# Kernel optimization log

Measured on AMD Instinct MI355X. Metric: run time of the kernel, lower is better.

The kernel has to match this reference:

```python
import jax, jax.numpy as jnp
import numpy as np

B, T, C, NH = 2, 128, 384, 6
H = 768          # memory MLP hidden (expansion=2)
P, M = 4, 16     # persistent + long-term memory tokens; prefix_len = P+M
LR, MOM, DECAY = 0.01, 0.9, 0.001

def setup_inputs() -> dict:
    key = jax.random.key(0)
    ks = jax.random.split(key, 12)
    s = 0.02
    return {
        'x':          jax.random.normal(ks[0], (B, T, C), jnp.float32),
        'c_attn_w':   jax.random.normal(ks[1], (C, 3 * C), jnp.float32) * s,
        'c_attn_b':   jnp.zeros((3 * C,), jnp.float32),
        'c_proj_w':   jax.random.normal(ks[2], (C, C), jnp.float32) * s,
        'c_proj_b':   jnp.zeros((C,), jnp.float32),
        'ln1_g': jnp.ones((C,), jnp.float32), 'ln1_b': jnp.zeros((C,), jnp.float32),
        'ln2_g': jnp.ones((C,), jnp.float32), 'ln2_b': jnp.zeros((C,), jnp.float32),
        'fc_w':       jax.random.normal(ks[3], (C, 4 * C), jnp.float32) * s,
        'fc_b':       jnp.zeros((4 * C,), jnp.float32),
        'pr_w':       jax.random.normal(ks[4], (4 * C, C), jnp.float32) * s,
        'pr_b':       jnp.zeros((C,), jnp.float32),
        'mem_w1':     jax.random.normal(ks[5], (C, H), jnp.float32) * s,
        'mem_w2':     jax.random.normal(ks[6], (H, C), jnp.float32) * s,
        'wk':         jax.random.normal(ks[7], (C, C), jnp.float32) * s,
        'wv':         jax.random.normal(ks[8], (C, C), jnp.float32) * s,
        'mem_queries': jax.random.normal(ks[9], (M, C), jnp.float32) * s,
        'persist':    jax.random.normal(ks[10], (P, C), jnp.float32) * s,
    }

def _ln(x, g, b):
    mu = jnp.mean(x, -1, keepdims=True)
    var = jnp.mean((x - mu) ** 2, -1, keepdims=True)
    return (x - mu) * jax.lax.rsqrt(var + 1e-5) * g + b

def _scan_log(gates, tokens):
    # x[t] = gate[t]*x[t-1] + token[t] via log-cumsum trick (scan axis = 1)
    while gates.ndim < tokens.ndim:
        gates = gates[..., None]
    g = jnp.clip(gates, 1e-7, 1.0 - 1e-7)
    lc = jnp.cumsum(jnp.log(g), axis=1)
    return jnp.cumsum(tokens * jnp.exp(-lc), axis=1) * jnp.exp(lc)

def _forward(x, c_attn_w, c_attn_b, c_proj_w, c_proj_b, ln1_g, ln1_b, ln2_g, ln2_b,
             fc_w, fc_b, pr_w, pr_b, mem_w1, mem_w2, wk, wv, mem_queries, persist):
    b = x.shape[0]
    hd = C // NH
    PL = P + M
    xn = _ln(x, ln1_g, ln1_b)
    # --- retrieve long-term memory tokens with previous-segment memory weights ---
    retr = jax.nn.silu(mem_queries @ mem_w1) @ mem_w2              # [M, C]
    pref = jnp.concatenate([persist, retr], axis=0)                # [PL, C]
    seq = jnp.concatenate([jnp.broadcast_to(pref, (b, PL, C)), xn], axis=1)  # [b, t, C]
    t = seq.shape[1]
    # --- prefix-LM masked attention ---
    qkv = seq @ c_attn_w + c_attn_b
    q, k, v = jnp.split(qkv, 3, axis=-1)
    def heads(z):
        return z.reshape(b, t, NH, hd).transpose(0, 2, 1, 3)       # [b, nh, t, hd]
    q, k, v = heads(q), heads(k), heads(v)
    sc = jnp.einsum('bhqd,bhkd->bhqk', q, k) / np.float32(np.sqrt(hd))
    idx = jnp.arange(t)
    kp = idx < PL  # key in prefix
    # prefix_lm_mask: key_in_prefix OR (both in suffix AND causal)
    allowed = kp[None, :] | ((~kp[:, None]) & (~kp[None, :]) & (idx[:, None] >= idx[None, :]))
    sc = jnp.where(allowed, sc, -jnp.inf)
    y = jnp.einsum('bhqk,bhkd->bhqd', jax.nn.softmax(sc, axis=-1), v)
    y = y.transpose(0, 2, 1, 3).reshape(b, t, C) @ c_proj_w + c_proj_b
    h1 = x + y[:, PL:, :]                                          # suffix (segment) outputs
    h2n = _ln(h1, ln2_g, ln2_b)
    h2 = h1 + (jax.nn.gelu(h2n @ fc_w + fc_b) @ pr_w + pr_b)
    # --- Titans neural memory update (per-token grads + momentum/decay scans) ---
    km = xn @ wk                                                   # [b, T, C]
    vm = xn @ wv
    hh = km @ mem_w1                                               # [b, T, H]
    a = jax.nn.silu(hh)
    err = a @ mem_w2 - vm                                          # [b, T, C]
    dw2 = jnp.einsum('bth,btc->bthc', a, err)                      # [b, T, H, C]
    sg = jax.nn.sigmoid(hh)
    dh = (err @ mem_w2.T) * (sg * (1.0 + hh * (1.0 - sg)))         # silu'
    dw1 = jnp.einsum('btc,bth->btch', km, dh)                      # [b, T, C, H]
    gm = jnp.full((b, T), MOM, x.dtype)
    scale = -(LR * (1.0 - MOM))
    m1 = _scan_log(gm, scale * dw1)
    m2 = _scan_log(gm, scale * dw2)
    def upd(w0, m):  # W[t] = (1-decay)*W[t-1] + m[t], W[-1] = w0
        toks = jnp.concatenate([jnp.broadcast_to(w0, (b,) + w0.shape)[:, None], m], axis=1)
        g = jnp.concatenate([jnp.ones((b, 1), x.dtype),
                             jnp.full((b, T), 1.0 - DECAY, x.dtype)], axis=1)
        return _scan_log(g, toks)[:, -1]
    w1f = upd(mem_w1, m1)                                          # [b, C, H]
    w2f = upd(mem_w2, m2)                                          # [b, H, C]
    # --- combine block output with updated-memory retrieval ---
    mem_out = jnp.einsum('bth,bhc->btc',
                         jax.nn.silu(jnp.einsum('btc,bch->bth', h2, w1f)), w2f)
    return h2 + mem_out

def reference(x, c_attn_w, c_attn_b, c_proj_w, c_proj_b, ln1_g, ln1_b, ln2_g, ln2_b,
              fc_w, fc_b, pr_w, pr_b, mem_w1, mem_w2, wk, wv, mem_queries, persist):
    return _forward(x, c_attn_w, c_attn_b, c_proj_w, c_proj_b, ln1_g, ln1_b, ln2_g, ln2_b,
                    fc_w, fc_b, pr_w, pr_b, mem_w1, mem_w2, wk, wv, mem_queries, persist)
```

## Files before the change

kernel.cpp:

```cpp
#include <hip/hip_runtime.h>
#include <math.h>

#define B_ 2
#define T_ 128
#define Cc 384
#define NH_ 6
#define HD 64
#define Hh 768
#define P_ 4
#define M_ 16
#define PL_ 20
#define TT 148

typedef unsigned short u16;
typedef short short8 __attribute__((ext_vector_type(8)));
typedef float f32x4 __attribute__((ext_vector_type(4)));

__device__ __forceinline__ u16 f2bf(float f) {
  unsigned int u = __float_as_uint(f);
  u += 0x7FFFu + ((u >> 16) & 1u);
  return (u16)(u >> 16);
}
__device__ __forceinline__ float siluf(float v) { return v / (1.f + expf(-v)); }
__device__ __forceinline__ float geluf(float v) {
  float x3 = v*v*v;
  return 0.5f*v*(1.f + tanhf(0.7978845608028654f*(v + 0.044715f*x3)));
}
template<int ACT> __device__ __forceinline__ float act_apply(float v) {
  if (ACT == 1) return geluf(v);
  if (ACT == 2) return siluf(v);
  return v;
}
__device__ __forceinline__ float coef_f(int k) {
  float e = (float)(T_ - k);
  return (exp2f(e * -0.00144342f) - exp2f(e * -0.15200310f)) * (1.0f/0.099f);
}
__device__ __forceinline__ void st_tr4(u16* dst, float v0, float v1, float v2, float v3) {
  union { u16 u[4]; uint2 d; } q;
  q.u[0]=f2bf(v0); q.u[1]=f2bf(v1); q.u[2]=f2bf(v2); q.u[3]=f2bf(v3);
  *(uint2*)dst = q.d;
}
__device__ __forceinline__ float wave_sum(float s) {
  #pragma unroll
  for (int off = 32; off; off >>= 1) s += __shfl_xor(s, off);
  return s;
}

struct Prm {
  const float *x,*c_attn_w,*c_attn_b,*c_proj_w,*c_proj_b,*ln1_g,*ln1_b,*ln2_g,*ln2_b,
              *fc_w,*fc_b,*pr_w,*pr_b,*mem_w1,*mem_w2,*wk,*wv,*mem_q,*persist;
  float *qkv,*vmb,*h1,*h2,*hhb,*outp;
  u16 *cattnT,*cprojT,*wkT,*wvT,*fcT,*prT,*w1tr,*w2tr,*w2pl,*memq,*hid,*seqb,*yb,*h2n,
      *fco,*h2b,*kmb,*kmTc,*ab,*abTc,*errB,*errT,*dhT,*w1fT,*w2fT,*ub;
  float scale, dpow;
};

template<int KSTEPS>
__device__ __forceinline__ void mfma_core(const u16* __restrict__ A,
    const u16* __restrict__ BT, int M, int mBase, int nBase, float (*red)[64][36])
{
  const long K = (long)KSTEPS * 128;
  int l = threadIdx.x & 63, w = threadIdx.x >> 6;
  int lr = l & 15, kg = l >> 4;
  long r0 = (long)min(mBase + lr, M - 1);
  long r1 = (long)min(mBase + 16 + lr, M - 1);
  long c0 = nBase + lr;
  long ko = (long)w * KSTEPS * 32 + kg * 8;
  const u16* pa0 = A + r0*K + ko;
  const u16* pa1 = A + r1*K + ko;
  const u16* pb0 = BT + c0*K + ko;
  const u16* pb1 = BT + (c0+16)*K + ko;
  const u16* pb2 = BT + (c0+32)*K + ko;
  const u16* pb3 = BT + (c0+48)*K + ko;
  f32x4 acc[2][4] = {};
  short8 a0 = *(const short8*)pa0, a1 = *(const short8*)pa1;
  short8 b0 = *(const short8*)pb0, b1 = *(const short8*)pb1;
  short8 b2 = *(const short8*)pb2, b3 = *(const short8*)pb3;
  #pragma unroll
  for (int t = 0; t < KSTEPS; ++t) {
    short8 xa0=a0, xa1=a1, xb0=b0, xb1=b1, xb2=b2, xb3=b3;
    if (t+1 < KSTEPS) {
      int o = (t+1)*32;
      a0 = *(const short8*)(pa0+o); a1 = *(const short8*)(pa1+o);
      b0 = *(const short8*)(pb0+o); b1 = *(const short8*)(pb1+o);
      b2 = *(const short8*)(pb2+o); b3 = *(const short8*)(pb3+o);
    }
    acc[0][0] = __builtin_amdgcn_mfma_f32_16x16x32_bf16(xa0, xb0, acc[0][0], 0,0,0);
    acc[0][1] = __builtin_amdgcn_mfma_f32_16x16x32_bf16(xa0, xb1, acc[0][1], 0,0,0);
    acc[0][2] = __builtin_amdgcn_mfma_f32_16x16x32_bf16(xa0, xb2, acc[0][2], 0,0,0);
    acc[0][3] = __builtin_amdgcn_mfma_f32_16x16x32_bf16(xa0, xb3, acc[0][3], 0,0,0);
    acc[1][0] = __builtin_amdgcn_mfma_f32_16x16x32_bf16(xa1, xb0, acc[1][0], 0,0,0);
    acc[1][1] = __builtin_amdgcn_mfma_f32_16x16x32_bf16(xa1, xb1, acc[1][1], 0,0,0);
    acc[1][2] = __builtin_amdgcn_mfma_f32_16x16x32_bf16(xa1, xb2, acc[1][2], 0,0,0);
    acc[1][3] = __builtin_amdgcn_mfma_f32_16x16x32_bf16(xa1, xb3, acc[1][3], 0,0,0);
  }
  #pragma unroll
  for (int i = 0; i < 2; ++i)
    #pragma unroll
    for (int j = 0; j < 4; ++j)
      *(f32x4*)&red[w][j*16 + lr][i*16 + kg*4] = acc[i][j];
  __syncthreads();
}

__device__ __forceinline__ void reduce8(float (*red)[64][36], float v[8], int& row0, int& col) {
  int tid = threadIdx.x;
  col = tid & 63;
  row0 = (tid >> 6) * 8;
  #pragma unroll
  for (int q = 0; q < 2; ++q) {
    f32x4 s = *(f32x4*)&red[0][col][row0 + q*4];
    s += *(f32x4*)&red[1][col][row0 + q*4];
    s += *(f32x4*)&red[2][col][row0 + q*4];
    s += *(f32x4*)&red[3][col][row0 + q*4];
    v[q*4+0] = s[0]; v[q*4+1] = s[1]; v[q*4+2] = s[2]; v[q*4+3] = s[3];
  }
}

template<int KSTEPS, int ACT, bool BIAS, bool RES, bool STF, bool STB, bool STTR>
__device__ __forceinline__ void gemm_task(const u16* A, const u16* BT,
    const float* bias, const float* res, float rscale,
    float* outF, u16* outB, u16* outT, int M, int N,
    int xx, int yy, float (*red)[64][36])
{
  int mBase = yy*32, nBase = xx*64;
  mfma_core<KSTEPS>(A, BT, M, mBase, nBase, red);
  float v[8]; int row0, col;
  reduce8(red, v, row0, col);
  int c = nBase + col;
  float bv = BIAS ? bias[c] : 0.f;
  #pragma unroll
  for (int q = 0; q < 8; ++q) {
    int r = mBase + row0 + q;
    float val = act_apply<ACT>(v[q] + bv);
    if (RES && r < M) val += rscale * res[(long)r*N + c];
    v[q] = val;
    if (r < M) {
      if (STF) outF[(long)r*N + c] = val;
      if (STB) outB[(long)r*N + c] = f2bf(val);
    }
  }
  if (STTR) {
    #pragma unroll
    for (int q = 0; q < 2; ++q) {
      int r = mBase + row0 + q*4;
      if (r < M) {
        int zz = r >> 7, t0 = r & 127;
        st_tr4(&outT[((long)zz*N + c)*128 + t0], v[q*4], v[q*4+1], v[q*4+2], v[q*4+3]);
      }
    }
  }
}

__global__ __launch_bounds__(256)
void k0_prep(Prm p)
{
  __shared__ float lds[4160];
  const int t = blockIdx.x;
  const int tid = threadIdx.x, w = tid >> 6, lane = tid & 63;
  if (t < 648) {
    const float* src; u16* dst; int K, N, tile;
    int b = t;
    if (b < 108)      { src=p.c_attn_w; dst=p.cattnT; K=384;  N=1152; tile=b; }
    else if (b < 144) { src=p.c_proj_w; dst=p.cprojT; K=384;  N=384;  tile=b-108; }
    else if (b < 180) { src=p.wk;       dst=p.wkT;    K=384;  N=384;  tile=b-144; }
    else if (b < 216) { src=p.wv;       dst=p.wvT;    K=384;  N=384;  tile=b-180; }
    else if (b < 360) { src=p.fc_w;     dst=p.fcT;    K=384;  N=1536; tile=b-216; }
    else if (b < 504) { src=p.pr_w;     dst=p.prT;    K=1536; N=384;  tile=b-360; }
    else if (b < 576) { src=p.mem_w1;   dst=p.w1tr;   K=384;  N=768;  tile=b-504; }
    else              { src=p.mem_w2;   dst=p.w2tr;   K=768;  N=384;  tile=b-576; }
    int ntx = N >> 6;
    int n0 = (tile % ntx) << 6, k0 = (tile / ntx) << 6;
    float (*fl)[65] = reinterpret_cast<float(*)[65]>(lds);
    int rr = tid >> 4, c4 = (tid & 15) << 2;
    #pragma unroll
    for (int i = 0; i < 4; ++i) {
      int row = rr + i*16;
      float4 vv = *(const float4*)&src[(long)(k0 + row)*N + n0 + c4];
      fl[row][c4] = vv.x; fl[row][c4+1] = vv.y; fl[row][c4+2] = vv.z; fl[row][c4+3] = vv.w;
    }
    __syncthreads();
    #pragma unroll
    for (int i = 0; i < 4; ++i) {
      int nrow = rr + i*16;
      st_tr4(&dst[(long)(n0 + nrow)*K + k0 + c4],
             fl[c4][nrow], fl[c4+1][nrow], fl[c4+2][nrow], fl[c4+3][nrow]);
    }
  } else if (t < 944) {
    int i = (t - 648)*256 + tid;
    if (i < 73728) {
      float4 v = *(const float4*)&p.mem_w2[(long)i*4];
      st_tr4(&p.w2pl[(long)i*4], v.x, v.y, v.z, v.w);
    } else if (i < 73728 + 1536) {
      int j = i - 73728;
      float4 v = *(const float4*)&p.mem_q[(long)j*4];
      st_tr4(&p.memq[(long)j*4], v.x, v.y, v.z, v.w);
    } else if (i < 73728 + 1536 + 384) {
      int j = i - 73728 - 1536;
      float4 v = *(const float4*)&p.persist[(long)j*4];
      st_tr4(&p.seqb[(long)j*4], v.x, v.y, v.z, v.w);
      st_tr4(&p.seqb[(long)TT*384 + j*4], v.x, v.y, v.z, v.w);
    }
  } else {
    int row = (t - 944)*4 + w;
    const float* src = p.x + (long)row*384;
    float v[6];
    #pragma unroll
    for (int i = 0; i < 6; ++i) v[i] = src[lane + i*64];
    float mu = wave_sum(v[0]+v[1]+v[2]+v[3]+v[4]+v[5]) * (1.f/384.f);
    float sq = 0.f;
    #pragma unroll
    for (int i = 0; i < 6; ++i) { float d = v[i]-mu; sq += d*d; }
    float rstd = rsqrtf(wave_sum(sq)*(1.f/384.f) + 1e-5f);
    u16* dst = p.seqb + ((long)(row >> 7)*TT + PL_ + (row & 127))*384;
    #pragma unroll
    for (int i = 0; i < 6; ++i) {
      int cc = lane + i*64;
      dst[cc] = f2bf((v[i]-mu)*rstd*p.ln1_g[cc] + p.ln1_b[cc]);
    }
  }
}

__global__ __launch_bounds__(256, 2)
void k0b_hid(Prm p)
{
  __shared__ float red[4][64][36];
  gemm_task<3,2,false,false,false,true,false>(p.memq, p.w1tr, nullptr, nullptr, 0.f,
      nullptr, p.hid, nullptr, 16, 768, blockIdx.x, 0, red);
}

__global__ __launch_bounds__(256, 2)
void k0c_retr(Prm p)
{
  __shared__ float red[4][64][36];
  int nBase = blockIdx.x*64;
  mfma_core<6>(p.hid, p.w2tr, 16, 0, nBase, red);
  float v[8]; int row0, col;
  reduce8(red, v, row0, col);
  int c = nBase + col;
  #pragma unroll
  for (int q = 0; q < 8; ++q) {
    int r = row0 + q;
    if (r < 16) {
      u16 bv = f2bf(v[q]);
      p.seqb[(long)(P_ + r)*384 + c] = bv;
      p.seqb[(long)(TT + P_ + r)*384 + c] = bv;
    }
  }
}

__global__ __launch_bounds__(256, 2)
void k1_qkv(Prm p)
{
  __shared__ float red[4][64][36];
  int t = blockIdx.x;
  int xx = t % 30, yy = t / 30;
  int nb = xx * 64;
  const u16* BT; int n0, seg;
  if (nb < 1152)      { BT = p.cattnT; n0 = nb;        seg = 0; }
  else if (nb < 1536) { BT = p.wkT;    n0 = nb - 1152; seg = 1; }
  else                { BT = p.wvT;    n0 = nb - 1536; seg = 2; }
  int mBase = yy*32;
  mfma_core<3>(p.seqb, BT, 296, mBase, n0, red);
  float v[8]; int row0, col;
  reduce8(red, v, row0, col);
  int c = n0 + col;
  if (seg == 0) {
    float bv = p.c_attn_b[c];
    #pragma unroll
    for (int q = 0; q < 8; ++q) {
      int r = mBase + row0 + q;
      if (r < 296) p.qkv[(long)r*1152 + c] = v[q] + bv;
    }
  } else if (seg == 1) {
    #pragma unroll
    for (int q = 0; q < 8; ++q) {
      int r = mBase + row0 + q;
      if (r < 296) {
        int z = r/148, tt2 = r - 20 - z*148;
        if (tt2 >= 0) p.kmb[((long)z*128 + tt2)*384 + c] = f2bf(v[q]);
      }
    }
    #pragma unroll
    for (int q = 0; q < 2; ++q) {
      int r = mBase + row0 + q*4;
      if (r < 296) {
        int z = r/148, t0 = r - 20 - z*148;
        if (t0 >= 0)
          st_tr4(&p.kmTc[((long)z*384 + c)*128 + t0],
                 v[q*4]*coef_f(t0), v[q*4+1]*coef_f(t0+1),
                 v[q*4+2]*coef_f(t0+2), v[q*4+3]*coef_f(t0+3));
      }
    }
  } else {
    #pragma unroll
    for (int q = 0; q < 8; ++q) {
      int r = mBase + row0 + q;
      if (r < 296) {
        int z = r/148, tt2 = r - 20 - z*148;
        if (tt2 >= 0) p.vmb[((long)z*128 + tt2)*384 + c] = v[q];
      }
    }
  }
}

__global__ __launch_bounds__(256, 2)
void k2_attn_hh(Prm p)
{
  __shared__ float red[4][64][36];
  const int t = blockIdx.x;
  const int tid = threadIdx.x, w = tid >> 6, lane = tid & 63;
  if (t < 384) {
    float* ldsf = (float*)red;
    float* qs = ldsf + w*64;
    float* pp = ldsf + 256 + w*152;
    int tt = t*4 + w;
    int qr = PL_ + (tt & 127);
    int h  = (tt >> 7) % 6;
    int b  = (tt / 768) & 1;
    const float* base = p.qkv + (long)b*TT*1152;
    qs[lane] = base[(long)qr*1152 + h*64 + lane];
    float mloc = -1e30f;
    for (int k = lane; k < TT; k += 64) {
      float s = -1e30f;
      if (k <= qr) {
        const float* kp = base + (long)k*1152 + 384 + h*64;
        float acc = 0.f;
        #pragma unroll
        for (int d = 0; d < 64; ++d) acc += qs[d]*kp[d];
        s = acc * 0.125f;
      }
      pp[k] = s;
      mloc = fmaxf(mloc, s);
    }
    #pragma unroll
    for (int off = 32; off; off >>= 1) mloc = fmaxf(mloc, __shfl_xor(mloc, off));
    float ssum = 0.f;
    for (int k = lane; k < TT; k += 64) {
      float e = (k <= qr) ? expf(pp[k] - mloc) : 0.f;
      pp[k] = e; ssum += e;
    }
    ssum = wave_sum(ssum);
    float inv = 1.f / ssum;
    float acc = 0.f;
    const float* vb = base + 768 + h*64 + lane;
    int k = 0;
    for (; k + 4 <= qr + 1; k += 4)
      acc += pp[k]*vb[(long)k*1152] + pp[k+1]*vb[(long)(k+1)*1152]
           + pp[k+2]*vb[(long)(k+2)*1152] + pp[k+3]*vb[(long)(k+3)*1152];
    for (; k <= qr; ++k) acc += pp[k]*vb[(long)k*1152];
    p.yb[((long)b*128 + (tt & 127))*384 + h*64 + lane] = f2bf(acc * inv);
  } else {
    int tt2 = t - 384;
    int xx = tt2 % 12, yy = tt2 / 12;
    int mBase = yy*32, nBase = xx*64;
    mfma_core<3>(p.kmb, p.w1tr, 256, mBase, nBase, red);
    float v[8]; int row0, col;
    reduce8(red, v, row0, col);
    int c = nBase + col;
    float s8[8];
    #pragma unroll
    for (int q = 0; q < 8; ++q) {
      int r = mBase + row0 + q;
      p.hhb[(long)r*768 + c] = v[q];
      s8[q] = siluf(v[q]);
      p.ab[(long)r*768 + c] = f2bf(s8[q]);
    }
    #pragma unroll
    for (int q = 0; q < 2; ++q) {
      int r = mBase + row0 + q*4;
      int zz = r >> 7, t0 = r & 127;
      st_tr4(&p.abTc[((long)zz*768 + c)*128 + t0],
             s8[q*4]*coef_f(t0), s8[q*4+1]*coef_f(t0+1),
             s8[q*4+2]*coef_f(t0+2), s8[q*4+3]*coef_f(t0+3));
    }
  }
}

__global__ __launch_bounds__(256, 2)
void k3_h1err(Prm p)
{
  __shared__ float red[4][64][36];
  int t = blockIdx.x;
  if (t < 48) {
    gemm_task<3,0,true,true,true,false,false>(p.yb, p.cprojT, p.c_proj_b, p.x, 1.f,
        p.h1, nullptr, nullptr, 256, 384, t % 6, t / 6, red);
  } else {
    int tt2 = t - 48;
    gemm_task<6,0,false,true,false,true,true>(p.ab, p.w2tr, nullptr, p.vmb, -1.f,
        nullptr, p.errB, p.errT, 256, 384, tt2 % 6, tt2 / 6, red);
  }
}

__global__ __launch_bounds__(256, 2)
void k4_ln2dh(Prm p)
{
  __shared__ float red[4][64][36];
  int t = blockIdx.x;
  const int tid = threadIdx.x, w = tid >> 6, lane = tid & 63;
  if (t < 64) {
    int row = t*4 + w;
    const float* src = p.h1 + (long)row*384;
    float v[6];
    #pragma unroll
    for (int i = 0; i < 6; ++i) v[i] = src[lane + i*64];
    float mu = wave_sum(v[0]+v[1]+v[2]+v[3]+v[4]+v[5]) * (1.f/384.f);
    float sq = 0.f;
    #pragma unroll
    for (int i = 0; i < 6; ++i) { float d = v[i]-mu; sq += d*d; }
    float rstd = rsqrtf(wave_sum(sq)*(1.f/384.f) + 1e-5f);
    u16* dst = p.h2n + (long)row*384;
    #pragma unroll
    for (int i = 0; i < 6; ++i) {
      int cc = lane + i*64;
      dst[cc] = f2bf((v[i]-mu)*rstd*p.ln2_g[cc] + p.ln2_b[cc]);
    }
  } else {
    int tt2 = t - 64;
    int xx = tt2 % 12, yy = tt2 / 12;
    int mBase = yy*32, nBase = xx*64;
    mfma_core<3>(p.errB, p.w2pl, 256, mBase, nBase, red);
    float v[8]; int row0, col;
    reduce8(red, v, row0, col);
    int c = nBase + col;
    #pragma unroll
    for (int q = 0; q < 8; ++q) {
      int r = mBase + row0 + q;
      float h = p.hhb[(long)r*768 + c];
      float sg = 1.f/(1.f + expf(-h));
      v[q] = v[q] * (sg*(1.f + h*(1.f - sg)));
    }
    #pragma unroll
    for (int q = 0; q < 2; ++q) {
      int r = mBase + row0 + q*4;
      int zz = r >> 7, t0 = r & 127;
      st_tr4(&p.dhT[((long)zz*768 + c)*128 + t0], v[q*4], v[q*4+1], v[q*4+2], v[q*4+3]);
    }
  }
}

__global__ __launch_bounds__(256, 2)
void k5_fcowupd(Prm p)
{
  __shared__ float red[4][64][36];
  int t = blockIdx.x;
  if (t < 192) {
    gemm_task<3,1,true,false,false,true,false>(p.h2n, p.fcT, p.fc_b, nullptr, 0.f,
        nullptr, p.fco, nullptr, 256, 1536, t % 24, t / 24, red);
  } else {
    const u16 *A, *BT; const float* W0; u16* Oz; int M, N, xx, yy, z;
    if (t < 480) {
      int tt2 = t - 192;
      xx = tt2 % 12; yy = (tt2 / 12) % 12; z = tt2 / 144;
      M = 384; N = 768;
      A = p.kmTc + (long)z*M*128; BT = p.dhT + (long)z*N*128;
      W0 = p.mem_w1; Oz = p.w1fT + (long)z*M*N;
    } else {
      int tt2 = t - 480;
      xx = tt2 % 6; yy = (tt2 / 6) % 24; z = tt2 / 144;
      M = 768; N = 384;
      A = p.abTc + (long)z*M*128; BT = p.errT + (long)z*N*128;
      W0 = p.mem_w2; Oz = p.w2fT + (long)z*M*N;
    }
    int mBase = yy*32, nBase = xx*64;
    mfma_core<1>(A, BT, M, mBase, nBase, red);
    float v[8]; int row0, col;
    reduce8(red, v, row0, col);
    int c = nBase + col;
    #pragma unroll
    for (int q = 0; q < 8; ++q) {
      int r = mBase + row0 + q;
      v[q] = p.dpow*W0[(long)r*N + c] + p.scale*v[q];
    }
    int r0 = mBase + row0;
    st_tr4(&Oz[(long)c*M + r0],     v[0], v[1], v[2], v[3]);
    st_tr4(&Oz[(long)c*M + r0 + 4], v[4], v[5], v[6], v[7]);
  }
}

__global__ __launch_bounds__(256, 2)
void k6_h2(Prm p)
{
  __shared__ float red[4][64][36];
  int t = blockIdx.x;
  gemm_task<12,0,true,true,true,true,false>(p.fco, p.prT, p.pr_b, p.h1, 1.f,
      p.h2, p.h2b, nullptr, 256, 384, t % 6, t / 6, red);
}

__global__ __launch_bounds__(256, 2)
void k7_ub(Prm p)
{
  __shared__ float red[4][64][36];
  int t = blockIdx.x;
  int z = t / 48, rr = t % 48;
  gemm_task<3,2,false,false,false,true,false>(
      p.h2b + (long)z*128*384, p.w1fT + (long)z*768*384, nullptr, nullptr, 0.f,
      nullptr, p.ub + (long)z*128*768, nullptr, 128, 768, rr % 12, rr / 12, red);
}

__global__ __launch_bounds__(256, 2)
void k8_out(Prm p)
{
  __shared__ float red[4][64][36];
  int t = blockIdx.x;
  int z = t / 24, rr = t % 24;
  gemm_task<6,0,false,true,true,false,false>(
      p.ub + (long)z*128*768, p.w2fT + (long)z*384*768, nullptr,
      p.h2 + (long)z*128*384, 1.f,
      p.outp + (long)z*128*384, nullptr, nullptr, 128, 384, rr % 6, rr / 6, red);
}

extern "C" void kernel_launch(void* const* d_in, const int* in_sizes, int n_in,
                              void* d_out, int out_size, void* d_ws, size_t ws_size,
                              hipStream_t stream)
{
  Prm p;
  p.x        = (const float*)d_in[0];
  p.c_attn_w = (const float*)d_in[1];
  p.c_attn_b = (const float*)d_in[2];
  p.c_proj_w = (const float*)d_in[3];
  p.c_proj_b = (const float*)d_in[4];
  p.ln1_g    = (const float*)d_in[5];
  p.ln1_b    = (const float*)d_in[6];
  p.ln2_g    = (const float*)d_in[7];
  p.ln2_b    = (const float*)d_in[8];
  p.fc_w     = (const float*)d_in[9];
  p.fc_b     = (const float*)d_in[10];
  p.pr_w     = (const float*)d_in[11];
  p.pr_b     = (const float*)d_in[12];
  p.mem_w1   = (const float*)d_in[13];
  p.mem_w2   = (const float*)d_in[14];
  p.wk       = (const float*)d_in[15];
  p.wv       = (const float*)d_in[16];
  p.mem_q    = (const float*)d_in[17];
  p.persist  = (const float*)d_in[18];

  float* f = (float*)d_ws;
  p.qkv = f;            f += 296L*1152;
  p.vmb = f;            f += 256L*384;
  p.h1  = f;            f += 256L*384;
  p.h2  = f;            f += 256L*384;
  p.hhb = f;            f += 256L*768;
  u16* b = (u16*)f;
  p.cattnT = b;  b += 1152L*384;
  p.cprojT = b;  b += 384L*384;
  p.wkT    = b;  b += 384L*384;
  p.wvT    = b;  b += 384L*384;
  p.fcT    = b;  b += 1536L*384;
  p.prT    = b;  b += 384L*1536;
  p.w1tr   = b;  b += 768L*384;
  p.w2tr   = b;  b += 384L*768;
  p.w2pl   = b;  b += 768L*384;
  p.memq   = b;  b += 16L*384;
  p.hid    = b;  b += 16L*768;
  p.seqb   = b;  b += 2L*TT*384;
  p.yb     = b;  b += 256L*384;
  p.h2n    = b;  b += 256L*384;
  p.fco    = b;  b += 256L*1536;
  p.h2b    = b;  b += 256L*384;
  p.kmb    = b;  b += 256L*384;
  p.kmTc   = b;  b += 2L*384*128;
  p.ab     = b;  b += 256L*768;
  p.abTc   = b;  b += 2L*768*128;
  p.errB   = b;  b += 256L*384;
  p.errT   = b;  b += 2L*384*128;
  p.dhT    = b;  b += 2L*768*128;
  p.w1fT   = b;  b += 2L*768*384;
  p.w2fT   = b;  b += 2L*384*768;
  p.ub     = b;  b += 2L*128*768;
  p.outp   = (float*)d_out;
  p.dpow   = powf(0.999f, 128.f);
  p.scale  = -0.001f;

  hipLaunchKernelGGL(k0_prep,    dim3(1008), dim3(256), 0, stream, p);
  hipLaunchKernelGGL(k0b_hid,    dim3(12),   dim3(256), 0, stream, p);
  hipLaunchKernelGGL(k0c_retr,   dim3(6),    dim3(256), 0, stream, p);
  hipLaunchKernelGGL(k1_qkv,     dim3(300),  dim3(256), 0, stream, p);
  hipLaunchKernelGGL(k2_attn_hh, dim3(480),  dim3(256), 0, stream, p);
  hipLaunchKernelGGL(k3_h1err,   dim3(96),   dim3(256), 0, stream, p);
  hipLaunchKernelGGL(k4_ln2dh,   dim3(160),  dim3(256), 0, stream, p);
  hipLaunchKernelGGL(k5_fcowupd, dim3(768),  dim3(256), 0, stream, p);
  hipLaunchKernelGGL(k6_h2,      dim3(48),   dim3(256), 0, stream, p);
  hipLaunchKernelGGL(k7_ub,      dim3(96),   dim3(256), 0, stream, p);
  hipLaunchKernelGGL(k8_out,     dim3(48),   dim3(256), 0, stream, p);
}
```

Before: 92.76 us.

## Fuse all stage kernels into one persistent kernel with grid barriers

Replaces eleven separate kernel launches with a single persistent kernel of 256 blocks. Each former kernel becomes a grid-stride loop over tasks, and the stages are separated by a software global barrier built on atomic counters kept in the workspace. This removes per-launch overhead and inter-kernel gaps. In exchange, the wide stages run with fewer blocks and more serial iterations per block, and the barriers spin on global atomics. Correctness also depends on all 256 blocks being resident at the same time.

After: 351.0 us. 3.78x slower.

```diff
diff --git a/kernel.cpp b/kernel.cpp
--- a/kernel.cpp
+++ b/kernel.cpp
@@ -11,6 +11,7 @@
 #define M_ 16
 #define PL_ 20
 #define TT 148
+#define GRID 256
 
 typedef unsigned short u16;
 typedef short short8 __attribute__((ext_vector_type(8)));
@@ -44,6 +45,24 @@
   #pragma unroll
   for (int off = 32; off; off >>= 1) s += __shfl_xor(s, off);
   return s;
+}
+
+__device__ __forceinline__ void gbar(unsigned* cnt, unsigned* gen) {
+  __syncthreads();
+  if (threadIdx.x == 0) {
+    __threadfence();
+    unsigned g = __hip_atomic_load(gen, __ATOMIC_RELAXED, __HIP_MEMORY_SCOPE_AGENT);
+    unsigned old = __hip_atomic_fetch_add(cnt, 1u, __ATOMIC_RELAXED, __HIP_MEMORY_SCOPE_AGENT);
+    if (old == GRID - 1u) {
+      __hip_atomic_store(cnt, 0u, __ATOMIC_RELAXED, __HIP_MEMORY_SCOPE_AGENT);
+      __hip_atomic_store(gen, g + 1u, __ATOMIC_RELEASE, __HIP_MEMORY_SCOPE_AGENT);
+    } else {
+      while (__hip_atomic_load(gen, __ATOMIC_RELAXED, __HIP_MEMORY_SCOPE_AGENT) == g)
+        __builtin_amdgcn_s_sleep(8);
+    }
+    __threadfence();
+  }
+  __syncthreads();
 }
 
 struct Prm {
@@ -52,6 +71,7 @@
   float *qkv,*vmb,*h1,*h2,*hhb,*outp;
   u16 *cattnT,*cprojT,*wkT,*wvT,*fcT,*prT,*w1tr,*w2tr,*w2pl,*memq,*hid,*seqb,*yb,*h2n,
       *fco,*h2b,*kmb,*kmTc,*ab,*abTc,*errB,*errT,*dhT,*w1fT,*w2fT,*ub;
+  unsigned *bcnt,*bgen;
   float scale, dpow;
 };
 
@@ -149,364 +169,344 @@
       }
     }
   }
-}
-
-__global__ __launch_bounds__(256)
-void k0_prep(Prm p)
+  __syncthreads();
+}
+
+__global__ __launch_bounds__(256, 2)
+void mega_k(Prm p)
 {
-  __shared__ float lds[4160];
-  const int t = blockIdx.x;
+  __shared__ float lds[9216];
+  float (*red)[64][36] = reinterpret_cast<float(*)[64][36]>(lds);
+  float* ldsf = lds;
+  const int bid = blockIdx.x;
   const int tid = threadIdx.x, w = tid >> 6, lane = tid & 63;
-  if (t < 648) {
-    const float* src; u16* dst; int K, N, tile;
-    int b = t;
-    if (b < 108)      { src=p.c_attn_w; dst=p.cattnT; K=384;  N=1152; tile=b; }
-    else if (b < 144) { src=p.c_proj_w; dst=p.cprojT; K=384;  N=384;  tile=b-108; }
-    else if (b < 180) { src=p.wk;       dst=p.wkT;    K=384;  N=384;  tile=b-144; }
-    else if (b < 216) { src=p.wv;       dst=p.wvT;    K=384;  N=384;  tile=b-180; }
-    else if (b < 360) { src=p.fc_w;     dst=p.fcT;    K=384;  N=1536; tile=b-216; }
-    else if (b < 504) { src=p.pr_w;     dst=p.prT;    K=1536; N=384;  tile=b-360; }
-    else if (b < 576) { src=p.mem_w1;   dst=p.w1tr;   K=384;  N=768;  tile=b-504; }
-    else              { src=p.mem_w2;   dst=p.w2tr;   K=768;  N=384;  tile=b-576; }
-    int ntx = N >> 6;
-    int n0 = (tile % ntx) << 6, k0 = (tile / ntx) << 6;
-    float (*fl)[65] = reinterpret_cast<float(*)[65]>(lds);
-    int rr = tid >> 4, c4 = (tid & 15) << 2;
-    #pragma unroll
-    for (int i = 0; i < 4; ++i) {
-      int row = rr + i*16;
-      float4 vv = *(const float4*)&src[(long)(k0 + row)*N + n0 + c4];
-      fl[row][c4] = vv.x; fl[row][c4+1] = vv.y; fl[row][c4+2] = vv.z; fl[row][c4+3] = vv.w;
+
+  for (int t = bid; t < 1008; t += GRID) {
+    if (t < 648) {
+      const float* src; u16* dst; int K, N, tile;
+      int b = t;
+      if (b < 108)      { src=p.c_attn_w; dst=p.cattnT; K=384;  N=1152; tile=b; }
+      else if (b < 144) { src=p.c_proj_w; dst=p.cprojT; K=384;  N=384;  tile=b-108; }
+      else if (b < 180) { src=p.wk;       dst=p.wkT;    K=384;  N=384;  tile=b-144; }
+      else if (b < 216) { src=p.wv;       dst=p.wvT;    K=384;  N=384;  tile=b-180; }
+      else if (b < 360) { src=p.fc_w;     dst=p.fcT;    K=384;  N=1536; tile=b-216; }
+      else if (b < 504) { src=p.pr_w;     dst=p.prT;    K=1536; N=384;  tile=b-360; }
+      else if (b < 576) { src=p.mem_w1;   dst=p.w1tr;   K=384;  N=768;  tile=b-504; }
+      else              { src=p.mem_w2;   dst=p.w2tr;   K=768;  N=384;  tile=b-576; }
+      int ntx = N >> 6;
+      int n0 = (tile % ntx) << 6, k0 = (tile / ntx) << 6;
+      float (*fl)[65] = reinterpret_cast<float(*)[65]>(lds);
+      int rr = tid >> 4, c4 = (tid & 15) << 2;
+      #pragma unroll
+      for (int i = 0; i < 4; ++i) {
+        int row = rr + i*16;
+        float4 vv = *(const float4*)&src[(long)(k0 + row)*N + n0 + c4];
+        fl[row][c4] = vv.x; fl[row][c4+1] = vv.y; fl[row][c4+2] = vv.z; fl[row][c4+3] = vv.w;
+      }
+      __syncthreads();
+      #pragma unroll
+      for (int i = 0; i < 4; ++i) {
+        int nrow = rr + i*16;
+        st_tr4(&dst[(long)(n0 + nrow)*K + k0 + c4],
+               fl[c4][nrow], fl[c4+1][nrow], fl[c4+2][nrow], fl[c4+3][nrow]);
+      }
+    } else if (t < 944) {
+      int i = (t - 648)*256 + tid;
+      if (i < 73728) {
+        float4 v = *(const float4*)&p.mem_w2[(long)i*4];
+        st_tr4(&p.w2pl[(long)i*4], v.x, v.y, v.z, v.w);
+      } else if (i < 73728 + 1536) {
+        int j = i - 73728;
+        float4 v = *(const float4*)&p.mem_q[(long)j*4];
+        st_tr4(&p.memq[(long)j*4], v.x, v.y, v.z, v.w);
+      } else if (i < 73728 + 1536 + 384) {
+        int j = i - 73728 - 1536;
+        float4 v = *(const float4*)&p.persist[(long)j*4];
+        st_tr4(&p.seqb[(long)j*4], v.x, v.y, v.z, v.w);
+        st_tr4(&p.seqb[(long)TT*384 + j*4], v.x, v.y, v.z, v.w);
+      }
+    } else {
+      int row = (t - 944)*4 + w;
+      const float* src = p.x + (long)row*384;
+      float v[6];
+      #pragma unroll
+      for (int i = 0; i < 6; ++i) v[i] = src[lane + i*64];
+      float mu = wave_sum(v[0]+v[1]+v[2]+v[3]+v[4]+v[5]) * (1.f/384.f);
+      float sq = 0.f;
+      #pragma unroll
+      for (int i = 0; i < 6; ++i) { float d = v[i]-mu; sq += d*d; }
+      float rstd = rsqrtf(wave_sum(sq)*(1.f/384.f) + 1e-5f);
+      u16* dst = p.seqb + ((long)(row >> 7)*TT + PL_ + (row & 127))*384;
+      #pragma unroll
+      for (int i = 0; i < 6; ++i) {
+        int cc = lane + i*64;
+        dst[cc] = f2bf((v[i]-mu)*rstd*p.ln1_g[cc] + p.ln1_b[cc]);
+      }
     }
     __syncthreads();
-    #pragma unroll
-    for (int i = 0; i < 4; ++i) {
-      int nrow = rr + i*16;
-      st_tr4(&dst[(long)(n0 + nrow)*K + k0 + c4],
-             fl[c4][nrow], fl[c4+1][nrow], fl[c4+2][nrow], fl[c4+3][nrow]);
-    }
-  } else if (t < 944) {
-    int i = (t - 648)*256 + tid;
-    if (i < 73728) {
-      float4 v = *(const float4*)&p.mem_w2[(long)i*4];
-      st_tr4(&p.w2pl[(long)i*4], v.x, v.y, v.z, v.w);
-    } else if (i < 73728 + 1536) {
-      int j = i - 73728;
-      float4 v = *(const float4*)&p.mem_q[(long)j*4];
-      st_tr4(&p.memq[(long)j*4], v.x, v.y, v.z, v.w);
-    } else if (i < 73728 + 1536 + 384) {
-      int j = i - 73728 - 1536;
-      float4 v = *(const float4*)&p.persist[(long)j*4];
-      st_tr4(&p.seqb[(long)j*4], v.x, v.y, v.z, v.w);
-      st_tr4(&p.seqb[(long)TT*384 + j*4], v.x, v.y, v.z, v.w);
-    }
-  } else {
-    int row = (t - 944)*4 + w;
-    const float* src = p.x + (long)row*384;
-    float v[6];
-    #pragma unroll
-    for (int i = 0; i < 6; ++i) v[i] = src[lane + i*64];
-    float mu = wave_sum(v[0]+v[1]+v[2]+v[3]+v[4]+v[5]) * (1.f/384.f);
-    float sq = 0.f;
-    #pragma unroll
-    for (int i = 0; i < 6; ++i) { float d = v[i]-mu; sq += d*d; }
-    float rstd = rsqrtf(wave_sum(sq)*(1.f/384.f) + 1e-5f);
-    u16* dst = p.seqb + ((long)(row >> 7)*TT + PL_ + (row & 127))*384;
-    #pragma unroll
-    for (int i = 0; i < 6; ++i) {
-      int cc = lane + i*64;
-      dst[cc] = f2bf((v[i]-mu)*rstd*p.ln1_g[cc] + p.ln1_b[cc]);
-    }
-  }
-}
-
-__global__ __launch_bounds__(256, 2)
-void k0b_hid(Prm p)
-{
-  __shared__ float red[4][64][36];
-  gemm_task<3,2,false,false,false,true,false>(p.memq, p.w1tr, nullptr, nullptr, 0.f,
-      nullptr, p.hid, nullptr, 16, 768, blockIdx.x, 0, red);
-}
-
-__global__ __launch_bounds__(256, 2)
-void k0c_retr(Prm p)
-{
-  __shared__ float red[4][64][36];
-  int nBase = blockIdx.x*64;
-  mfma_core<6>(p.hid, p.w2tr, 16, 0, nBase, red);
-  float v[8]; int row0, col;
-  reduce8(red, v, row0, col);
-  int c = nBase + col;
-  #pragma unroll
-  for (int q = 0; q < 8; ++q) {
-    int r = row0 + q;
-    if (r < 16) {
-      u16 bv = f2bf(v[q]);
-      p.seqb[(long)(P_ + r)*384 + c] = bv;
-      p.seqb[(long)(TT + P_ + r)*384 + c] = bv;
-    }
-  }
-}
-
-__global__ __launch_bounds__(256, 2)
-void k1_qkv(Prm p)
-{
-  __shared__ float red[4][64][36];
-  int t = blockIdx.x;
-  int xx = t % 30, yy = t / 30;
-  int nb = xx * 64;
-  const u16* BT; int n0, seg;
-  if (nb < 1152)      { BT = p.cattnT; n0 = nb;        seg = 0; }
-  else if (nb < 1536) { BT = p.wkT;    n0 = nb - 1152; seg = 1; }
-  else                { BT = p.wvT;    n0 = nb - 1536; seg = 2; }
-  int mBase = yy*32;
-  mfma_core<3>(p.seqb, BT, 296, mBase, n0, red);
-  float v[8]; int row0, col;
-  reduce8(red, v, row0, col);
-  int c = n0 + col;
-  if (seg == 0) {
-    float bv = p.c_attn_b[c];
-    #pragma unroll
-    for (int q = 0; q < 8; ++q) {
-      int r = mBase + row0 + q;
-      if (r < 296) p.qkv[(long)r*1152 + c] = v[q] + bv;
-    }
-  } else if (seg == 1) {
-    #pragma unroll
-    for (int q = 0; q < 8; ++q) {
-      int r = mBase + row0 + q;
-      if (r < 296) {
-        int z = r/148, tt2 = r - 20 - z*148;
-        if (tt2 >= 0) p.kmb[((long)z*128 + tt2)*384 + c] = f2bf(v[q]);
-      }
-    }
-    #pragma unroll
-    for (int q = 0; q < 2; ++q) {
-      int r = mBase + row0 + q*4;
-      if (r < 296) {
-        int z = r/148, t0 = r - 20 - z*148;
-        if (t0 >= 0)
-          st_tr4(&p.kmTc[((long)z*384 + c)*128 + t0],
-                 v[q*4]*coef_f(t0), v[q*4+1]*coef_f(t0+1),
-                 v[q*4+2]*coef_f(t0+2), v[q*4+3]*coef_f(t0+3));
-      }
-    }
-  } else {
-    #pragma unroll
-    for (int q = 0; q < 8; ++q) {
-      int r = mBase + row0 + q;
-      if (r < 296) {
-        int z = r/148, tt2 = r - 20 - z*148;
-        if (tt2 >= 0) p.vmb[((long)z*128 + tt2)*384 + c] = v[q];
-      }
-    }
-  }
-}
-
-__global__ __launch_bounds__(256, 2)
-void k2_attn_hh(Prm p)
-{
-  __shared__ float red[4][64][36];
-  const int t = blockIdx.x;
-  const int tid = threadIdx.x, w = tid >> 6, lane = tid & 63;
-  if (t < 384) {
-    float* ldsf = (float*)red;
-    float* qs = ldsf + w*64;
-    float* pp = ldsf + 256 + w*152;
-    int tt = t*4 + w;
-    int qr = PL_ + (tt & 127);
-    int h  = (tt >> 7) % 6;
-    int b  = (tt / 768) & 1;
-    const float* base = p.qkv + (long)b*TT*1152;
-    qs[lane] = base[(long)qr*1152 + h*64 + lane];
-    float mloc = -1e30f;
-    for (int k = lane; k < TT; k += 64) {
-      float s = -1e30f;
-      if (k <= qr) {
-        const float* kp = base + (long)k*1152 + 384 + h*64;
-        float acc = 0.f;
-        #pragma unroll
-        for (int d = 0; d < 64; ++d) acc += qs[d]*kp[d];
-        s = acc * 0.125f;
-      }
-      pp[k] = s;
-      mloc = fmaxf(mloc, s);
-    }
-    #pragma unroll
-    for (int off = 32; off; off >>= 1) mloc = fmaxf(mloc, __shfl_xor(mloc, off));
-    float ssum = 0.f;
-    for (int k = lane; k < TT; k += 64) {
-      float e = (k <= qr) ? expf(pp[k] - mloc) : 0.f;
-      pp[k] = e; ssum += e;
-    }
-    ssum = wave_sum(ssum);
-    float inv = 1.f / ssum;
-    float acc = 0.f;
-    const float* vb = base + 768 + h*64 + lane;
-    int k = 0;
-    for (; k + 4 <= qr + 1; k += 4)
-      acc += pp[k]*vb[(long)k*1152] + pp[k+1]*vb[(long)(k+1)*1152]
-           + pp[k+2]*vb[(long)(k+2)*1152] + pp[k+3]*vb[(long)(k+3)*1152];
-    for (; k <= qr; ++k) acc += pp[k]*vb[(long)k*1152];
-    p.yb[((long)b*128 + (tt & 127))*384 + h*64 + lane] = f2bf(acc * inv);
-  } else {
-    int tt2 = t - 384;
-    int xx = tt2 % 12, yy = tt2 / 12;
-    int mBase = yy*32, nBase = xx*64;
-    mfma_core<3>(p.kmb, p.w1tr, 256, mBase, nBase, red);
-    float v[8]; int row0, col;
-    reduce8(red, v, row0, col);
-    int c = nBase + col;
-    float s8[8];
-    #pragma unroll
-    for (int q = 0; q < 8; ++q) {
-      int r = mBase + row0 + q;
-      p.hhb[(long)r*768 + c] = v[q];
-      s8[q] = siluf(v[q]);
-      p.ab[(long)r*768 + c] = f2bf(s8[q]);
-    }
-    #pragma unroll
-    for (int q = 0; q < 2; ++q) {
-      int r = mBase + row0 + q*4;
-      int zz = r >> 7, t0 = r & 127;
-      st_tr4(&p.abTc[((long)zz*768 + c)*128 + t0],
-             s8[q*4]*coef_f(t0), s8[q*4+1]*coef_f(t0+1),
-             s8[q*4+2]*coef_f(t0+2), s8[q*4+3]*coef_f(t0+3));
-    }
-  }
-}
-
-__global__ __launch_bounds__(256, 2)
-void k3_h1err(Prm p)
-{
-  __shared__ float red[4][64][36];
-  int t = blockIdx.x;
-  if (t < 48) {
-    gemm_task<3,0,true,true,true,false,false>(p.yb, p.cprojT, p.c_proj_b, p.x, 1.f,
-        p.h1, nullptr, nullptr, 256, 384, t % 6, t / 6, red);
-  } else {
-    int tt2 = t - 48;
-    gemm_task<6,0,false,true,false,true,true>(p.ab, p.w2tr, nullptr, p.vmb, -1.f,
-        nullptr, p.errB, p.errT, 256, 384, tt2 % 6, tt2 / 6, red);
-  }
-}
-
-__global__ __launch_bounds__(256, 2)
-void k4_ln2dh(Prm p)
-{
-  __shared__ float red[4][64][36];
-  int t = blockIdx.x;
-  const int tid = threadIdx.x, w = tid >> 6, lane = tid & 63;
-  if (t < 64) {
-    int row = t*4 + w;
-    const float* src = p.h1 + (long)row*384;
-    float v[6];
-    #pragma unroll
-    for (int i = 0; i < 6; ++i) v[i] = src[lane + i*64];
-    float mu = wave_sum(v[0]+v[1]+v[2]+v[3]+v[4]+v[5]) * (1.f/384.f);
-    float sq = 0.f;
-    #pragma unroll
-    for (int i = 0; i < 6; ++i) { float d = v[i]-mu; sq += d*d; }
-    float rstd = rsqrtf(wave_sum(sq)*(1.f/384.f) + 1e-5f);
-    u16* dst = p.h2n + (long)row*384;
-    #pragma unroll
-    for (int i = 0; i < 6; ++i) {
-      int cc = lane + i*64;
-      dst[cc] = f2bf((v[i]-mu)*rstd*p.ln2_g[cc] + p.ln2_b[cc]);
-    }
-  } else {
-    int tt2 = t - 64;
-    int xx = tt2 % 12, yy = tt2 / 12;
-    int mBase = yy*32, nBase = xx*64;
-    mfma_core<3>(p.errB, p.w2pl, 256, mBase, nBase, red);
+  }
+  gbar(p.bcnt, p.bgen);
+
+  for (int t = bid; t < 12; t += GRID)
+    gemm_task<3,2,false,false,false,true,false>(p.memq, p.w1tr, nullptr, nullptr, 0.f,
+        nullptr, p.hid, nullptr, 16, 768, t, 0, red);
+  gbar(p.bcnt, p.bgen);
+
+  for (int t = bid; t < 6; t += GRID) {
+    int nBase = t*64;
+    mfma_core<6>(p.hid, p.w2tr, 16, 0, nBase, red);
     float v[8]; int row0, col;
     reduce8(red, v, row0, col);
     int c = nBase + col;
     #pragma unroll
     for (int q = 0; q < 8; ++q) {
-      int r = mBase + row0 + q;
-      float h = p.hhb[(long)r*768 + c];
-      float sg = 1.f/(1.f + expf(-h));
-      v[q] = v[q] * (sg*(1.f + h*(1.f - sg)));
-    }
-    #pragma unroll
-    for (int q = 0; q < 2; ++q) {
-      int r = mBase + row0 + q*4;
-      int zz = r >> 7, t0 = r & 127;
-      st_tr4(&p.dhT[((long)zz*768 + c)*128 + t0], v[q*4], v[q*4+1], v[q*4+2], v[q*4+3]);
-    }
-  }
-}
-
-__global__ __launch_bounds__(256, 2)
-void k5_fcowupd(Prm p)
-{
-  __shared__ float red[4][64][36];
-  int t = blockIdx.x;
-  if (t < 192) {
-    gemm_task<3,1,true,false,false,true,false>(p.h2n, p.fcT, p.fc_b, nullptr, 0.f,
-        nullptr, p.fco, nullptr, 256, 1536, t % 24, t / 24, red);
-  } else {
-    const u16 *A, *BT; const float* W0; u16* Oz; int M, N, xx, yy, z;
-    if (t < 480) {
-      int tt2 = t - 192;
-      xx = tt2 % 12; yy = (tt2 / 12) % 12; z = tt2 / 144;
-      M = 384; N = 768;
-      A = p.kmTc + (long)z*M*128; BT = p.dhT + (long)z*N*128;
-      W0 = p.mem_w1; Oz = p.w1fT + (long)z*M*N;
-    } else {
-      int tt2 = t - 480;
-      xx = tt2 % 6; yy = (tt2 / 6) % 24; z = tt2 / 144;
-      M = 768; N = 384;
-      A = p.abTc + (long)z*M*128; BT = p.errT + (long)z*N*128;
-      W0 = p.mem_w2; Oz = p.w2fT + (long)z*M*N;
-    }
-    int mBase = yy*32, nBase = xx*64;
-    mfma_core<1>(A, BT, M, mBase, nBase, red);
+      int r = row0 + q;
+      if (r < 16) {
+        u16 bv = f2bf(v[q]);
+        p.seqb[(long)(P_ + r)*384 + c] = bv;
+        p.seqb[(long)(TT + P_ + r)*384 + c] = bv;
+      }
+    }
+    __syncthreads();
+  }
+  gbar(p.bcnt, p.bgen);
+
+  for (int t = bid; t < 300; t += GRID) {
+    int xx = t % 30, yy = t / 30;
+    int nb = xx * 64;
+    const u16* BT; int n0, seg;
+    if (nb < 1152)      { BT = p.cattnT; n0 = nb;        seg = 0; }
+    else if (nb < 1536) { BT = p.wkT;    n0 = nb - 1152; seg = 1; }
+    else                { BT = p.wvT;    n0 = nb - 1536; seg = 2; }
+    int mBase = yy*32;
+    mfma_core<3>(p.seqb, BT, 296, mBase, n0, red);
     float v[8]; int row0, col;
     reduce8(red, v, row0, col);
-    int c = nBase + col;
-    #pragma unroll
-    for (int q = 0; q < 8; ++q) {
-      int r = mBase + row0 + q;
-      v[q] = p.dpow*W0[(long)r*N + c] + p.scale*v[q];
-    }
-    int r0 = mBase + row0;
-    st_tr4(&Oz[(long)c*M + r0],     v[0], v[1], v[2], v[3]);
-    st_tr4(&Oz[(long)c*M + r0 + 4], v[4], v[5], v[6], v[7]);
-  }
-}
-
-__global__ __launch_bounds__(256, 2)
-void k6_h2(Prm p)
-{
-  __shared__ float red[4][64][36];
-  int t = blockIdx.x;
-  gemm_task<12,0,true,true,true,true,false>(p.fco, p.prT, p.pr_b, p.h1, 1.f,
-      p.h2, p.h2b, nullptr, 256, 384, t % 6, t / 6, red);
-}
-
-__global__ __launch_bounds__(256, 2)
-void k7_ub(Prm p)
-{
-  __shared__ float red[4][64][36];
-  int t = blockIdx.x;
-  int z = t / 48, rr = t % 48;
-  gemm_task<3,2,false,false,false,true,false>(
-      p.h2b + (long)z*128*384, p.w1fT + (long)z*768*384, nullptr, nullptr, 0.f,
-      nullptr, p.ub + (long)z*128*768, nullptr, 128, 768, rr % 12, rr / 12, red);
-}
-
-__global__ __launch_bounds__(256, 2)
-void k8_out(Prm p)
-{
-  __shared__ float red[4][64][36];
-  int t = blockIdx.x;
-  int z = t / 24, rr = t % 24;
-  gemm_task<6,0,false,true,true,false,false>(
-      p.ub + (long)z*128*768, p.w2fT + (long)z*384*768, nullptr,
-      p.h2 + (long)z*128*384, 1.f,
-      p.outp + (long)z*128*384, nullptr, nullptr, 128, 384, rr % 6, rr / 6, red);
+    int c = n0 + col;
+    if (seg == 0) {
+      float bv = p.c_attn_b[c];
+      #pragma unroll
+      for (int q = 0; q < 8; ++q) {
+        int r = mBase + row0 + q;
+        if (r < 296) p.qkv[(long)r*1152 + c] = v[q] + bv;
+      }
+    } else if (seg == 1) {
+      #pragma unroll
+      for (int q = 0; q < 8; ++q) {
+        int r = mBase + row0 + q;
+        if (r < 296) {
+          int z = r/148, tt2 = r - 20 - z*148;
+          if (tt2 >= 0) p.kmb[((long)z*128 + tt2)*384 + c] = f2bf(v[q]);
+        }
+      }
+      #pragma unroll
+      for (int q = 0; q < 2; ++q) {
+        int r = mBase + row0 + q*4;
+        if (r < 296) {
+          int z = r/148, t0 = r - 20 - z*148;
+          if (t0 >= 0)
+            st_tr4(&p.kmTc[((long)z*384 + c)*128 + t0],
+                   v[q*4]*coef_f(t0), v[q*4+1]*coef_f(t0+1),
+                   v[q*4+2]*coef_f(t0+2), v[q*4+3]*coef_f(t0+3));
+        }
+      }
+    } else {
+      #pragma unroll
+      for (int q = 0; q < 8; ++q) {
+        int r = mBase + row0 + q;
+        if (r < 296) {
+          int z = r/148, tt2 = r - 20 - z*148;
+          if (tt2 >= 0) p.vmb[((long)z*128 + tt2)*384 + c] = v[q];
+        }
+      }
+    }
+    __syncthreads();
+  }
+  gbar(p.bcnt, p.bgen);
+
+  for (int t = bid; t < 480; t += GRID) {
+    if (t < 384) {
+      float* qs = ldsf + w*64;
+      float* pp = ldsf + 256 + w*152;
+      int tt = t*4 + w;
+      int qr = PL_ + (tt & 127);
+      int h  = (tt >> 7) % 6;
+      int b  = (tt / 768) & 1;
+      const float* base = p.qkv + (long)b*TT*1152;
+      qs[lane] = base[(long)qr*1152 + h*64 + lane];
+      float mloc = -1e30f;
+      for (int k = lane; k < TT; k += 64) {
+        float s = -1e30f;
+        if (k <= qr) {
+          const float* kp = base + (long)k*1152 + 384 + h*64;
+          float acc = 0.f;
+          #pragma unroll
+          for (int d = 0; d < 64; ++d) acc += qs[d]*kp[d];
+          s = acc * 0.125f;
+        }
+        pp[k] = s;
+        mloc = fmaxf(mloc, s);
+      }
+      #pragma unroll
+      for (int off = 32; off; off >>= 1) mloc = fmaxf(mloc, __shfl_xor(mloc, off));
+      float ssum = 0.f;
+      for (int k = lane; k < TT; k += 64) {
+        float e = (k <= qr) ? expf(pp[k] - mloc) : 0.f;
+        pp[k] = e; ssum += e;
+      }
+      ssum = wave_sum(ssum);
+      float inv = 1.f / ssum;
+      float acc = 0.f;
+      const float* vb = base + 768 + h*64 + lane;
+      int k = 0;
+      for (; k + 4 <= qr + 1; k += 4)
+        acc += pp[k]*vb[(long)k*1152] + pp[k+1]*vb[(long)(k+1)*1152]
+             + pp[k+2]*vb[(long)(k+2)*1152] + pp[k+3]*vb[(long)(k+3)*1152];
+      for (; k <= qr; ++k) acc += pp[k]*vb[(long)k*1152];
+      p.yb[((long)b*128 + (tt & 127))*384 + h*64 + lane] = f2bf(acc * inv);
+    } else {
+      int tt2 = t - 384;
+      int xx = tt2 % 12, yy = tt2 / 12;
+      int mBase = yy*32, nBase = xx*64;
+      mfma_core<3>(p.kmb, p.w1tr, 256, mBase, nBase, red);
+      float v[8]; int row0, col;
+      reduce8(red, v, row0, col);
+      int c = nBase + col;
+      float s8[8];
+      #pragma unroll
+      for (int q = 0; q < 8; ++q) {
+        int r = mBase + row0 + q;
+        p.hhb[(long)r*768 + c] = v[q];
+        s8[q] = siluf(v[q]);
+        p.ab[(long)r*768 + c] = f2bf(s8[q]);
+      }
+      #pragma unroll
+      for (int q = 0; q < 2; ++q) {
+        int r = mBase + row0 + q*4;
+        int zz = r >> 7, t0 = r & 127;
+        st_tr4(&p.abTc[((long)zz*768 + c)*128 + t0],
+               s8[q*4]*coef_f(t0), s8[q*4+1]*coef_f(t0+1),
+               s8[q*4+2]*coef_f(t0+2), s8[q*4+3]*coef_f(t0+3));
+      }
+    }
+    __syncthreads();
+  }
+  gbar(p.bcnt, p.bgen);
+
+  for (int t = bid; t < 96; t += GRID) {
+    if (t < 48)
+      gemm_task<3,0,true,true,true,false,false>(p.yb, p.cprojT, p.c_proj_b, p.x, 1.f,
+          p.h1, nullptr, nullptr, 256, 384, t % 6, t / 6, red);
+    else {
+      int tt2 = t - 48;
+      gemm_task<6,0,false,true,false,true,true>(p.ab, p.w2tr, nullptr, p.vmb, -1.f,
+          nullptr, p.errB, p.errT, 256, 384, tt2 % 6, tt2 / 6, red);
+    }
+  }
+  gbar(p.bcnt, p.bgen);
+
+  for (int t = bid; t < 160; t += GRID) {
+    if (t < 64) {
+      int row = t*4 + w;
+      const float* src = p.h1 + (long)row*384;
+      float v[6];
+      #pragma unroll
+      for (int i = 0; i < 6; ++i) v[i] = src[lane + i*64];
+      float mu = wave_sum(v[0]+v[1]+v[2]+v[3]+v[4]+v[5]) * (1.f/384.f);
+      float sq = 0.f;
+      #pragma unroll
+      for (int i = 0; i < 6; ++i) { float d = v[i]-mu; sq += d*d; }
+      float rstd = rsqrtf(wave_sum(sq)*(1.f/384.f) + 1e-5f);
+      u16* dst = p.h2n + (long)row*384;
+      #pragma unroll
+      for (int i = 0; i < 6; ++i) {
+        int cc = lane + i*64;
+        dst[cc] = f2bf((v[i]-mu)*rstd*p.ln2_g[cc] + p.ln2_b[cc]);
+      }
+      __syncthreads();
+    } else {
+      int tt2 = t - 64;
+      int xx = tt2 % 12, yy = tt2 / 12;
+      int mBase = yy*32, nBase = xx*64;
+      mfma_core<3>(p.errB, p.w2pl, 256, mBase, nBase, red);
+      float v[8]; int row0, col;
+      reduce8(red, v, row0, col);
+      int c = nBase + col;
+      #pragma unroll
+      for (int q = 0; q < 8; ++q) {
+        int r = mBase + row0 + q;
+        float h = p.hhb[(long)r*768 + c];
+        float sg = 1.f/(1.f + expf(-h));
+        v[q] = v[q] * (sg*(1.f + h*(1.f - sg)));
+      }
+      #pragma unroll
+      for (int q = 0; q < 2; ++q) {
+        int r = mBase + row0 + q*4;
+        int zz = r >> 7, t0 = r & 127;
+        st_tr4(&p.dhT[((long)zz*768 + c)*128 + t0], v[q*4], v[q*4+1], v[q*4+2], v[q*4+3]);
+      }
+      __syncthreads();
+    }
+  }
+  gbar(p.bcnt, p.bgen);
+
+  for (int t = bid; t < 768; t += GRID) {
+    if (t < 192)
+      gemm_task<3,1,true,false,false,true,false>(p.h2n, p.fcT, p.fc_b, nullptr, 0.f,
+          nullptr, p.fco, nullptr, 256, 1536, t % 24, t / 24, red);
+    else {
+      const u16 *A, *BT; const float* W0; u16* Oz; int M, N, xx, yy, z;
+      if (t < 480) {
+        int tt2 = t - 192;
+        xx = tt2 % 12; yy = (tt2 / 12) % 12; z = tt2 / 144;
+        M = 384; N = 768;
+        A = p.kmTc + (long)z*M*128; BT = p.dhT + (long)z*N*128;
+        W0 = p.mem_w1; Oz = p.w1fT + (long)z*M*N;
+      } else {
+        int tt2 = t - 480;
+        xx = tt2 % 6; yy = (tt2 / 6) % 24; z = tt2 / 144;
+        M = 768; N = 384;
+        A = p.abTc + (long)z*M*128; BT = p.errT + (long)z*N*128;
+        W0 = p.mem_w2; Oz = p.w2fT + (long)z*M*N;
+      }
+      int mBase = yy*32, nBase = xx*64;
+      mfma_core<1>(A, BT, M, mBase, nBase, red);
+      float v[8]; int row0, col;
+      reduce8(red, v, row0, col);
+      int c = nBase + col;
+      #pragma unroll
+      for (int q = 0; q < 8; ++q) {
+        int r = mBase + row0 + q;
+        v[q] = p.dpow*W0[(long)r*N + c] + p.scale*v[q];
+      }
+      int r0 = mBase + row0;
+      st_tr4(&Oz[(long)c*M + r0],     v[0], v[1], v[2], v[3]);
+      st_tr4(&Oz[(long)c*M + r0 + 4], v[4], v[5], v[6], v[7]);
+      __syncthreads();
+    }
+  }
+  gbar(p.bcnt, p.bgen);
+
+  for (int t = bid; t < 48; t += GRID)
+    gemm_task<12,0,true,true,true,true,false>(p.fco, p.prT, p.pr_b, p.h1, 1.f,
+        p.h2, p.h2b, nullptr, 256, 384, t % 6, t / 6, red);
+  gbar(p.bcnt, p.bgen);
+
+  for (int t = bid; t < 96; t += GRID) {
+    int z = t / 48, rr = t % 48;
+    gemm_task<3,2,false,false,false,true,false>(
+        p.h2b + (long)z*128*384, p.w1fT + (long)z*768*384, nullptr, nullptr, 0.f,
+        nullptr, p.ub + (long)z*128*768, nullptr, 128, 768, rr % 12, rr / 12, red);
+  }
+  gbar(p.bcnt, p.bgen);
+
+  for (int t = bid; t < 48; t += GRID) {
+    int z = t / 24, rr = t % 24;
+    gemm_task<6,0,false,true,true,false,false>(
+        p.ub + (long)z*128*768, p.w2fT + (long)z*384*768, nullptr,
+        p.h2 + (long)z*128*384, 1.f,
+        p.outp + (long)z*128*384, nullptr, nullptr, 128, 384, rr % 6, rr / 6, red);
+  }
 }
 
 extern "C" void kernel_launch(void* const* d_in, const int* in_sizes, int n_in,
@@ -534,7 +534,10 @@
   p.mem_q    = (const float*)d_in[17];
   p.persist  = (const float*)d_in[18];
 
-  float* f = (float*)d_ws;
+  p.bcnt = (unsigned*)d_ws;
+  p.bgen = p.bcnt + 1;
+
+  float* f = (float*)((char*)d_ws + 256);
   p.qkv = f;            f += 296L*1152;
   p.vmb = f;            f += 256L*384;
   p.h1  = f;            f += 256L*384;
@@ -571,15 +574,6 @@
   p.dpow   = powf(0.999f, 128.f);
   p.scale  = -0.001f;
 
-  hipLaunchKernelGGL(k0_prep,    dim3(1008), dim3(256), 0, stream, p);
-  hipLaunchKernelGGL(k0b_hid,    dim3(12),   dim3(256), 0, stream, p);
-  hipLaunchKernelGGL(k0c_retr,   dim3(6),    dim3(256), 0, stream, p);
-  hipLaunchKernelGGL(k1_qkv,     dim3(300),  dim3(256), 0, stream, p);
-  hipLaunchKernelGGL(k2_attn_hh, dim3(480),  dim3(256), 0, stream, p);
-  hipLaunchKernelGGL(k3_h1err,   dim3(96),   dim3(256), 0, stream, p);
-  hipLaunchKernelGGL(k4_ln2dh,   dim3(160),  dim3(256), 0, stream, p);
-  hipLaunchKernelGGL(k5_fcowupd, dim3(768),  dim3(256), 0, stream, p);
-  hipLaunchKernelGGL(k6_h2,      dim3(48),   dim3(256), 0, stream, p);
-  hipLaunchKernelGGL(k7_ub,      dim3(96),   dim3(256), 0, stream, p);
-  hipLaunchKernelGGL(k8_out,     dim3(48),   dim3(256), 0, stream, p);
-}
+  hipMemsetAsync(d_ws, 0, 256, stream);
+  hipLaunchKernelGGL(mega_k, dim3(GRID), dim3(256), 0, stream, p);
+}
```
